# Kernel optimization log

Measured on AMD Instinct MI355X. Metric: run time of the kernel, lower is better.

## Reference

```python
import jax, jax.numpy as jnp
import numpy as np

N_NODES = 100000
N_EDGES = 1600000
IN_DIM, HID_DIM, OUT_DIM = 128, 64, 64
NEG_SLOPE = 0.2


def _gat_layer(h_in, src, dst, W, a_src, a_dst, b, n_nodes):
    # h: [N, F_out]
    h = h_in @ W.T
    alpha_src = h @ a_src  # [N]
    alpha_dst = h @ a_dst  # [N]
    # per-edge raw attention logits (edge j->i: src=j, dst=i)
    e = jax.nn.leaky_relu(alpha_src[src] + alpha_dst[dst], NEG_SLOPE)  # [E]
    # segment softmax over incoming edges of each dst node
    m = jax.ops.segment_max(e, dst, num_segments=n_nodes)
    ex = jnp.exp(e - m[dst])
    denom = jax.ops.segment_sum(ex, dst, num_segments=n_nodes)
    alpha = ex / denom[dst]  # [E], denom > 0 thanks to self-loops
    out = jax.ops.segment_sum(h[src] * alpha[:, None], dst, num_segments=n_nodes)
    return out + b


def setup_inputs() -> dict:
    key = jax.random.key(0)
    ks = jax.random.split(key, 12)
    x = jax.random.normal(ks[0], (N_NODES, IN_DIM), dtype=jnp.float32)
    edge_index = jax.random.randint(ks[1], (2, N_EDGES), 0, N_NODES)
    edge_attr = jax.random.normal(ks[2], (N_EDGES, 1), dtype=jnp.float32)
    s1 = 1.0 / np.sqrt(IN_DIM)
    s2 = 1.0 / np.sqrt(HID_DIM)
    W1 = jax.random.normal(ks[3], (HID_DIM, IN_DIM), dtype=jnp.float32) * s1
    att_src1 = jax.random.normal(ks[4], (HID_DIM,), dtype=jnp.float32) * s2
    att_dst1 = jax.random.normal(ks[5], (HID_DIM,), dtype=jnp.float32) * s2
    b1 = jnp.zeros((HID_DIM,), dtype=jnp.float32)
    W2 = jax.random.normal(ks[6], (OUT_DIM, HID_DIM), dtype=jnp.float32) * s2
    att_src2 = jax.random.normal(ks[7], (OUT_DIM,), dtype=jnp.float32) * s2
    att_dst2 = jax.random.normal(ks[8], (OUT_DIM,), dtype=jnp.float32) * s2
    b2 = jnp.zeros((OUT_DIM,), dtype=jnp.float32)
    return {"x": x, "edge_index": edge_index, "edge_attr": edge_attr,
            "W1": W1, "att_src1": att_src1, "att_dst1": att_dst1, "b1": b1,
            "W2": W2, "att_src2": att_src2, "att_dst2": att_dst2, "b2": b2}


def reference(x, edge_index, edge_attr, W1, att_src1, att_dst1, b1,
              W2, att_src2, att_dst2, b2):
    n = x.shape[0]
    # add self-loops (PyG GATConv default); edge_attr unused (edge_dim=None)
    loop = jnp.arange(n, dtype=edge_index.dtype)
    src = jnp.concatenate([edge_index[0], loop])
    dst = jnp.concatenate([edge_index[1], loop])
    h = _gat_layer(x, src, dst, W1, att_src1, att_dst1, b1, n)
    h = jax.nn.relu(h)
    h = _gat_layer(h, src, dst, W2, att_src2, att_dst2, b2, n)
    # global_mean_pool with batch=None -> mean over all nodes, shape [1, F]
    return jnp.mean(h, axis=0, keepdims=True)
```

## Files before the change

kernel.cpp:

```cpp
#include <hip/hip_runtime.h>

#define NEG_SLOPE 0.2f
#define BSHIFT 6
#define NBMAX 2048
#define BCAP 1408
#define CHUNK 4096

typedef __attribute__((ext_vector_type(8))) short short8;
typedef __attribute__((ext_vector_type(4))) float f32x4;

__device__ __forceinline__ unsigned short f2b(float x) {
    unsigned u = __float_as_uint(x);
    u += 0x7fff + ((u >> 16) & 1);
    return (unsigned short)(u >> 16);
}
__device__ __forceinline__ float b2f(unsigned short u) {
    return __uint_as_float((unsigned)u << 16);
}

__global__ __launch_bounds__(256) void hist_kernel(
    const int* __restrict__ ei, int* __restrict__ hist, int E, int NB)
{
    __shared__ int cnt[NBMAX];
    const int tid = threadIdx.x;
    for (int i = tid; i < NB; i += 256) cnt[i] = 0;
    __syncthreads();
    const int start = blockIdx.x * CHUNK;
    const int end = min(start + CHUNK, E);
    for (int i = start + tid; i < end; i += 256)
        atomicAdd(&cnt[ei[E + i] >> BSHIFT], 1);
    __syncthreads();
    for (int i = tid; i < NB; i += 256)
        hist[(size_t)blockIdx.x * NB + i] = cnt[i];
}

__global__ __launch_bounds__(256) void colscan_kernel(
    int* __restrict__ hist, int* __restrict__ btotal, int NB, int NBLK)
{
    const int b = blockIdx.x * 256 + threadIdx.x;
    if (b >= NB) return;
    int run = 0;
    int blk = 0;
    for (; blk + 8 <= NBLK; blk += 8) {
        int w[8];
        #pragma unroll
        for (int j = 0; j < 8; ++j) w[j] = hist[(size_t)(blk + j) * NB + b];
        #pragma unroll
        for (int j = 0; j < 8; ++j) {
            hist[(size_t)(blk + j) * NB + b] = run;
            run += w[j];
        }
    }
    for (; blk < NBLK; ++blk) {
        int w = hist[(size_t)blk * NB + b];
        hist[(size_t)blk * NB + b] = run;
        run += w;
    }
    btotal[b] = run;
}

__global__ __launch_bounds__(256) void scatter_kernel(
    const int* __restrict__ ei, const int* __restrict__ hist,
    int* __restrict__ binned, int E, int NB)
{
    __shared__ int base[NBMAX], cnt2[NBMAX];
    const int tid = threadIdx.x;
    for (int i = tid; i < NB; i += 256) {
        base[i] = hist[(size_t)blockIdx.x * NB + i];
        cnt2[i] = 0;
    }
    __syncthreads();
    const int start = blockIdx.x * CHUNK;
    const int end = min(start + CHUNK, E);
    for (int i = start + tid; i < end; i += 256) {
        int s = ei[i], d = ei[E + i];
        int b = d >> BSHIFT;
        int r = base[b] + atomicAdd(&cnt2[b], 1);
        if (r < BCAP) binned[(size_t)b * BCAP + r] = (s << BSHIFT) | (d & 63);
    }
}

__global__ __launch_bounds__(256) void bscan_kernel(
    const int* __restrict__ btotal, int* __restrict__ bbase, int NB)
{
    __shared__ int lds[256];
    const int t = threadIdx.x;
    int v[8]; int s = 0;
    #pragma unroll
    for (int j = 0; j < 8; ++j) {
        int i = t * 8 + j;
        v[j] = (i < NB) ? min(btotal[i], BCAP) : 0;
        s += v[j];
    }
    lds[t] = s;
    __syncthreads();
    #pragma unroll
    for (int off = 1; off < 256; off <<= 1) {
        int x = (t >= off) ? lds[t - off] : 0;
        __syncthreads();
        lds[t] += x;
        __syncthreads();
    }
    int excl = (t > 0) ? lds[t - 1] : 0;
    #pragma unroll
    for (int j = 0; j < 8; ++j) {
        int i = t * 8 + j;
        if (i < NB) { bbase[i] = excl + 64 * i; excl += v[j]; }
    }
}

__global__ __launch_bounds__(256) void bucket_csr_kernel(
    const int* __restrict__ binned, const int* __restrict__ btotal,
    const int* __restrict__ bbase, int* __restrict__ row_ptr,
    int* __restrict__ esrc, int N)
{
    __shared__ int ldeg[64];
    __shared__ int lcur[64];
    const int b = blockIdx.x;
    const int tid = threadIdx.x;
    const int node0 = b << BSHIFT;
    const int cnt = min(btotal[b], BCAP);
    const int base_e = bbase[b];
    const int* bp = binned + (size_t)b * BCAP;

    if (tid < 64) ldeg[tid] = (node0 + tid < N) ? 1 : 0;
    __syncthreads();
    for (int i = tid; i < cnt; i += 256)
        atomicAdd(&ldeg[bp[i] & 63], 1);
    __syncthreads();
    if (tid < 64) {
        int v = ldeg[tid];
        int inc = v;
        #pragma unroll
        for (int off = 1; off < 64; off <<= 1) {
            int t2 = __shfl_up(inc, off, 64);
            if (tid >= off) inc += t2;
        }
        int excl = inc - v;
        int node = node0 + tid;
        if (node <= N) row_ptr[node] = base_e + excl;
        if (node < N) {
            esrc[base_e + excl] = node;
            lcur[tid] = base_e + excl + 1;
        }
    }
    __syncthreads();
    for (int i = tid; i < cnt; i += 256) {
        int v = bp[i];
        int pos = atomicAdd(&lcur[v & 63], 1);
        esrc[pos] = v >> BSHIFT;
    }
}

template<int K, bool BF16IN>
__global__ __launch_bounds__(256) void gemm_attn_kernel(
    const void* __restrict__ in_v, const float* __restrict__ W,
    const float* __restrict__ a_src, const float* __restrict__ a_dst,
    unsigned short* __restrict__ hb, float* __restrict__ asrc,
    float* __restrict__ adst, int N)
{
    constexpr int LDK = K + 8;
    __shared__ unsigned short xb[64 * LDK];
    __shared__ unsigned short wb[64 * LDK];
    __shared__ float avs[64], avd[64];

    const int tid = threadIdx.x;
    const int node0 = blockIdx.x * 64;
    const int w = tid >> 6;
    const int lane = tid & 63;
    const int col = lane & 15;
    const int quad = lane >> 4;

    if (tid < 64) { avs[tid] = a_src[tid]; avd[tid] = a_dst[tid]; }

    for (int i = tid; i < 64 * (K / 4); i += 256) {
        int r = i / (K / 4), c = i % (K / 4);
        float4 v = *(const float4*)&W[(size_t)r * K + 4 * c];
        *(ushort4*)&wb[r * LDK + 4 * c] =
            make_ushort4(f2b(v.x), f2b(v.y), f2b(v.z), f2b(v.w));
    }
    if (BF16IN) {
        const unsigned short* in = (const unsigned short*)in_v;
        for (int i = tid; i < 64 * (K / 8); i += 256) {
            int r = i / (K / 8), c = i % (K / 8);
            int node = node0 + r;
            ulonglong2 v = (node < N)
                ? *(const ulonglong2*)&in[(size_t)node * K + 8 * c]
                : make_ulonglong2(0ull, 0ull);
            *(ulonglong2*)&xb[r * LDK + 8 * c] = v;
        }
    } else {
        const float* in = (const float*)in_v;
        for (int i = tid; i < 64 * (K / 4); i += 256) {
            int r = i / (K / 4), c = i % (K / 4);
            int node = node0 + r;
            float4 v = (node < N) ? *(const float4*)&in[(size_t)node * K + 4 * c]
                                  : make_float4(0.f, 0.f, 0.f, 0.f);
            *(ushort4*)&xb[r * LDK + 4 * c] =
                make_ushort4(f2b(v.x), f2b(v.y), f2b(v.z), f2b(v.w));
        }
    }
    __syncthreads();

    f32x4 acc[4] = {f32x4{0,0,0,0}, f32x4{0,0,0,0}, f32x4{0,0,0,0}, f32x4{0,0,0,0}};
    #pragma unroll
    for (int kc = 0; kc < K / 32; ++kc) {
        short8 a = *(const short8*)&xb[(16 * w + col) * LDK + kc * 32 + quad * 8];
        #pragma unroll
        for (int j = 0; j < 4; ++j) {
            short8 b = *(const short8*)&wb[(16 * j + col) * LDK + kc * 32 + quad * 8];
            acc[j] = __builtin_amdgcn_mfma_f32_16x16x32_bf16(a, b, acc[j], 0, 0, 0);
        }
    }

    #pragma unroll
    for (int r = 0; r < 4; ++r) {
        const int node = node0 + 16 * w + quad * 4 + r;
        const bool valid = node < N;
        float vs = 0.f, vd = 0.f;
        #pragma unroll
        for (int j = 0; j < 4; ++j) {
            float hv = acc[j][r];
            int f = 16 * j + col;
            if (valid) hb[(size_t)node * 64 + f] = f2b(hv);
            vs = fmaf(hv, avs[f], vs);
            vd = fmaf(hv, avd[f], vd);
        }
        #pragma unroll
        for (int off = 8; off >= 1; off >>= 1) {
            vs += __shfl_down(vs, off, 16);
            vd += __shfl_down(vd, off, 16);
        }
        if (col == 0 && valid) { asrc[node] = vs; adst[node] = vd; }
    }
}

__global__ __launch_bounds__(256) void aggregate_csr_kernel(
    const int* __restrict__ row_ptr, const int* __restrict__ esrc,
    const float* __restrict__ asrc, const float* __restrict__ adst,
    const unsigned short* __restrict__ hb, const float* __restrict__ bias,
    unsigned short* __restrict__ gb, int N, int do_relu)
{
    const int node = (int)((blockIdx.x * 256 + threadIdx.x) >> 2);
    const int lane = threadIdx.x & 3;
    if (node >= N) return;
    const int beg = row_ptr[node];
    const int end = row_ptr[node + 1];
    const float ad = adst[node];
    const unsigned short* hbase = hb + lane * 16;

    float acc[16];
    #pragma unroll
    for (int k = 0; k < 16; ++k) acc[k] = 0.f;
    float wsum = 0.f;

    int p = beg;
    for (; p + 4 <= end; p += 4) {
        int s[4]; short8 r0[4], r1[4]; float l[4];
        #pragma unroll
        for (int j = 0; j < 4; ++j) s[j] = esrc[p + j];
        #pragma unroll
        for (int j = 0; j < 4; ++j) {
            const unsigned short* hp = hbase + (size_t)s[j] * 64;
            r0[j] = *(const short8*)hp;
            r1[j] = *(const short8*)(hp + 8);
        }
        #pragma unroll
        for (int j = 0; j < 4; ++j) l[j] = asrc[s[j]] + ad;
        #pragma unroll
        for (int j = 0; j < 4; ++j) {
            float ll = (l[j] > 0.f) ? l[j] : NEG_SLOPE * l[j];
            float w = __expf(ll);
            wsum += w;
            #pragma unroll
            for (int k = 0; k < 8; ++k)
                acc[k] = fmaf(w, b2f((unsigned short)r0[j][k]), acc[k]);
            #pragma unroll
            for (int k = 0; k < 8; ++k)
                acc[8 + k] = fmaf(w, b2f((unsigned short)r1[j][k]), acc[8 + k]);
        }
    }
    for (; p < end; ++p) {
        int s = esrc[p];
        const unsigned short* hp = hbase + (size_t)s * 64;
        short8 r0 = *(const short8*)hp;
        short8 r1 = *(const short8*)(hp + 8);
        float l = asrc[s] + ad;
        l = (l > 0.f) ? l : NEG_SLOPE * l;
        float w = __expf(l);
        wsum += w;
        #pragma unroll
        for (int k = 0; k < 8; ++k)
            acc[k] = fmaf(w, b2f((unsigned short)r0[k]), acc[k]);
        #pragma unroll
        for (int k = 0; k < 8; ++k)
            acc[8 + k] = fmaf(w, b2f((unsigned short)r1[k]), acc[8 + k]);
    }

    const float inv = 1.0f / wsum;
    short8 s0, s1;
    #pragma unroll
    for (int k = 0; k < 8; ++k) {
        float v0 = acc[k] * inv;
        float v1 = acc[8 + k] * inv;
        if (bias) { v0 += bias[lane * 16 + k]; v1 += bias[lane * 16 + 8 + k]; }
        if (do_relu) { v0 = fmaxf(v0, 0.f); v1 = fmaxf(v1, 0.f); }
        s0[k] = (short)f2b(v0);
        s1[k] = (short)f2b(v1);
    }
    unsigned short* gp = gb + (size_t)node * 64 + lane * 16;
    *(short8*)gp = s0;
    *(short8*)(gp + 8) = s1;
}

__global__ __launch_bounds__(256) void pool_kernel(
    const unsigned short* __restrict__ gb, const float* __restrict__ b2,
    float* __restrict__ out, int N)
{
    __shared__ float red[256];
    const int f = threadIdx.x & 63;
    const int sub = threadIdx.x >> 6;
    float acc = 0.f;
    for (int n = blockIdx.x * 4 + sub; n < N; n += gridDim.x * 4)
        acc += b2f(gb[(size_t)n * 64 + f]);
    red[threadIdx.x] = acc;
    __syncthreads();
    if (threadIdx.x < 64) {
        float s = red[f] + red[64 + f] + red[128 + f] + red[192 + f];
        atomicAdd(out + f, s * (1.0f / (float)N));
        if (blockIdx.x == 0) atomicAdd(out + f, b2[f]);
    }
}

extern "C" void kernel_launch(void* const* d_in, const int* in_sizes, int n_in,
                              void* d_out, int out_size, void* d_ws, size_t ws_size,
                              hipStream_t stream) {
    const float* x   = (const float*)d_in[0];
    const int*   ei  = (const int*)d_in[1];
    const float* W1  = (const float*)d_in[3];
    const float* as1 = (const float*)d_in[4];
    const float* ad1 = (const float*)d_in[5];
    const float* b1  = (const float*)d_in[6];
    const float* W2  = (const float*)d_in[7];
    const float* as2 = (const float*)d_in[8];
    const float* ad2 = (const float*)d_in[9];
    const float* b2  = (const float*)d_in[10];
    float* out = (float*)d_out;

    const int N = in_sizes[0] / 128;
    const int E = in_sizes[1] / 2;
    const int Etot = E + N;
    const int NB = (N + 63) >> BSHIFT;
    const int NBLK = (E + CHUNK - 1) / CHUNK;

    auto align4 = [](size_t v) { return (v + 3) & ~(size_t)3; };
    float* ws    = (float*)d_ws;
    size_t off = 0;
    unsigned short* hb = (unsigned short*)(ws + off); off += align4((size_t)N * 32);
    unsigned short* gb = (unsigned short*)(ws + off); off += align4((size_t)N * 32);
    float* asrc  = ws + off; off += align4(N);
    float* adst  = ws + off; off += align4(N);
    int* row_ptr = (int*)(ws + off); off += align4(N + 1);
    int* btotal  = (int*)(ws + off); off += NBMAX;
    int* bbase   = (int*)(ws + off); off += NBMAX;
    int* hist    = (int*)(ws + off); off += align4((size_t)NBLK * NB);
    int* esrc    = (int*)(ws + off); off += align4(Etot);
    int* binned  = (int*)gb;

    const int gemm_blocks = (N + 63) / 64;
    const int agg_blocks  = (int)(((size_t)N * 4 + 255) / 256);

    hipMemsetAsync(out, 0, 64 * sizeof(float), stream);

    hist_kernel<<<NBLK, 256, 0, stream>>>(ei, hist, E, NB);
    colscan_kernel<<<(NB + 255) / 256, 256, 0, stream>>>(hist, btotal, NB, NBLK);
    scatter_kernel<<<NBLK, 256, 0, stream>>>(ei, hist, binned, E, NB);
    bscan_kernel<<<1, 256, 0, stream>>>(btotal, bbase, NB);
    bucket_csr_kernel<<<NB, 256, 0, stream>>>(binned, btotal, bbase, row_ptr, esrc, N);

    gemm_attn_kernel<128, false><<<gemm_blocks, 256, 0, stream>>>(
        x, W1, as1, ad1, hb, asrc, adst, N);
    aggregate_csr_kernel<<<agg_blocks, 256, 0, stream>>>(
        row_ptr, esrc, asrc, adst, hb, b1, gb, N, 1);

    gemm_attn_kernel<64, true><<<gemm_blocks, 256, 0, stream>>>(
        gb, W2, as2, ad2, hb, asrc, adst, N);
    aggregate_csr_kernel<<<agg_blocks, 256, 0, stream>>>(
        row_ptr, esrc, asrc, adst, hb, nullptr, gb, N, 0);

    pool_kernel<<<512, 256, 0, stream>>>(gb, b2, out, N);
}
```

Before: 304.4 us.

## Parallelize column scan per wavefront, reorder scatter chunks, split aggregation edges

The column scan now gives each histogram column a 64-lane wavefront that runs a shuffle-based prefix scan, replacing one serial thread per column. The scatter kernel remaps block IDs so that blocks running at the same time handle chunks spread across the edge list. The aggregation kernel now uses two 4-lane groups per node that each take half of the incoming edges and combine their partial sums with an xor shuffle. Together these add parallelism and latency hiding to the preprocessing and to the gather-bound aggregation, at the cost of twice as many aggregation threads and a 16-value shuffle reduction per node.

Result: faster. 290.6 us (-4.5%).

```diff
diff --git a/kernel.cpp b/kernel.cpp
--- a/kernel.cpp
+++ b/kernel.cpp
@@ -37,26 +37,24 @@
 __global__ __launch_bounds__(256) void colscan_kernel(
     int* __restrict__ hist, int* __restrict__ btotal, int NB, int NBLK)
 {
-    const int b = blockIdx.x * 256 + threadIdx.x;
-    if (b >= NB) return;
+    const int col = (int)((blockIdx.x * 256 + threadIdx.x) >> 6);
+    const int ln  = threadIdx.x & 63;
+    if (col >= NB) return;
     int run = 0;
-    int blk = 0;
-    for (; blk + 8 <= NBLK; blk += 8) {
-        int w[8];
-        #pragma unroll
-        for (int j = 0; j < 8; ++j) w[j] = hist[(size_t)(blk + j) * NB + b];
-        #pragma unroll
-        for (int j = 0; j < 8; ++j) {
-            hist[(size_t)(blk + j) * NB + b] = run;
-            run += w[j];
-        }
-    }
-    for (; blk < NBLK; ++blk) {
-        int w = hist[(size_t)blk * NB + b];
-        hist[(size_t)blk * NB + b] = run;
-        run += w;
-    }
-    btotal[b] = run;
+    for (int r0 = 0; r0 < NBLK; r0 += 64) {
+        const int r = r0 + ln;
+        const bool ok = (r < NBLK);
+        int v = ok ? hist[(size_t)r * NB + col] : 0;
+        int inc = v;
+        #pragma unroll
+        for (int off = 1; off < 64; off <<= 1) {
+            int x = __shfl_up(inc, off, 64);
+            if (ln >= off) inc += x;
+        }
+        if (ok) hist[(size_t)r * NB + col] = run + inc - v;
+        run += __shfl(inc, 63, 64);
+    }
+    if (ln == 0) btotal[col] = run;
 }
 
 __global__ __launch_bounds__(256) void scatter_kernel(
@@ -64,13 +62,18 @@
     int* __restrict__ binned, int E, int NB)
 {
     __shared__ int base[NBMAX], cnt2[NBMAX];
+    const int nblk = gridDim.x;
+    const int q = nblk >> 3, rr = nblk & 7;
+    const int x = blockIdx.x & 7, k = blockIdx.x >> 3;
+    const int chunk = ((x < rr) ? x * (q + 1) : rr * (q + 1) + (x - rr) * q) + k;
+
     const int tid = threadIdx.x;
     for (int i = tid; i < NB; i += 256) {
-        base[i] = hist[(size_t)blockIdx.x * NB + i];
+        base[i] = hist[(size_t)chunk * NB + i];
         cnt2[i] = 0;
     }
     __syncthreads();
-    const int start = blockIdx.x * CHUNK;
+    const int start = chunk * CHUNK;
     const int end = min(start + CHUNK, E);
     for (int i = start + tid; i < end; i += 256) {
         int s = ei[i], d = ei[E + i];
@@ -241,11 +244,13 @@
     const unsigned short* __restrict__ hb, const float* __restrict__ bias,
     unsigned short* __restrict__ gb, int N, int do_relu)
 {
-    const int node = (int)((blockIdx.x * 256 + threadIdx.x) >> 2);
+    const int node = (int)((blockIdx.x * 256 + threadIdx.x) >> 3);
     const int lane = threadIdx.x & 3;
+    const int grp  = (threadIdx.x >> 2) & 1;
     if (node >= N) return;
     const int beg = row_ptr[node];
     const int end = row_ptr[node + 1];
+    const int mid = (beg + end + 1) >> 1;
     const float ad = adst[node];
     const unsigned short* hbase = hb + lane * 16;
 
@@ -254,8 +259,9 @@
     for (int k = 0; k < 16; ++k) acc[k] = 0.f;
     float wsum = 0.f;
 
-    int p = beg;
-    for (; p + 4 <= end; p += 4) {
+    int p = grp ? mid : beg;
+    const int pe = grp ? end : mid;
+    for (; p + 4 <= pe; p += 4) {
         int s[4]; short8 r0[4], r1[4]; float l[4];
         #pragma unroll
         for (int j = 0; j < 4; ++j) s[j] = esrc[p + j];
@@ -280,7 +286,7 @@
                 acc[8 + k] = fmaf(w, b2f((unsigned short)r1[j][k]), acc[8 + k]);
         }
     }
-    for (; p < end; ++p) {
+    for (; p < pe; ++p) {
         int s = esrc[p];
         const unsigned short* hp = hbase + (size_t)s * 64;
         short8 r0 = *(const short8*)hp;
@@ -296,6 +302,11 @@
         for (int k = 0; k < 8; ++k)
             acc[8 + k] = fmaf(w, b2f((unsigned short)r1[k]), acc[8 + k]);
     }
+
+    wsum += __shfl_xor(wsum, 4, 64);
+    #pragma unroll
+    for (int k = 0; k < 16; ++k) acc[k] += __shfl_xor(acc[k], 4, 64);
+    if (grp) return;
 
     const float inv = 1.0f / wsum;
     short8 s0, s1;
@@ -368,12 +379,12 @@
     int* binned  = (int*)gb;
 
     const int gemm_blocks = (N + 63) / 64;
-    const int agg_blocks  = (int)(((size_t)N * 4 + 255) / 256);
+    const int agg_blocks  = (int)(((size_t)N * 8 + 255) / 256);
 
     hipMemsetAsync(out, 0, 64 * sizeof(float), stream);
 
     hist_kernel<<<NBLK, 256, 0, stream>>>(ei, hist, E, NB);
-    colscan_kernel<<<(NB + 255) / 256, 256, 0, stream>>>(hist, btotal, NB, NBLK);
+    colscan_kernel<<<(NB * 64 + 255) / 256, 256, 0, stream>>>(hist, btotal, NB, NBLK);
     scatter_kernel<<<NBLK, 256, 0, stream>>>(ei, hist, binned, E, NB);
     bscan_kernel<<<1, 256, 0, stream>>>(btotal, bbase, NB);
     bucket_csr_kernel<<<NB, 256, 0, stream>>>(binned, btotal, bbase, row_ptr, esrc, N);
```
